# Optimization experiments

Measured on AMD Instinct MI355X. Metric: run time of the kernel, lower is better.

## Reference

```python
import jax, jax.numpy as jnp
import numpy as np

HEADS = 16
DIM_HEAD = 64
SCALE = DIM_HEAD ** -0.5


def setup_inputs() -> dict:
    key = jax.random.key(0)
    k1, k2, k3, k4 = jax.random.split(key, 4)
    b, n, dim = 2, 2048, 1024
    inner = HEADS * DIM_HEAD  # 1024
    x = jax.random.normal(k1, (b, n, dim), dtype=jnp.float32)
    # binary keep-mask (multiplicative, as in the original module)
    seq_mask = (jax.random.uniform(k2, (b, n)) < 0.9).astype(jnp.float32)
    # weights stored [in, out] (transpose of torch Linear layout)
    w_qkv = jax.random.normal(k3, (dim, inner * 3), dtype=jnp.float32) * (dim ** -0.5)
    w_out = jax.random.normal(k4, (inner, dim), dtype=jnp.float32) * (inner ** -0.5)
    return {"x": x, "seq_mask": seq_mask, "w_qkv": w_qkv, "w_out": w_out}


def reference(x, seq_mask, w_qkv, w_out):
    b, n, dim = x.shape
    qkv = x @ w_qkv                                   # [b, n, 3*inner]
    q, k, v = jnp.split(qkv, 3, axis=-1)
    split_heads = lambda t: t.reshape(b, n, HEADS, DIM_HEAD).transpose(0, 2, 1, 3)
    q, k, v = split_heads(q), split_heads(k), split_heads(v)  # [b, h, n, d]
    dots = jnp.einsum('bhid,bhjd->bhij', q, k) * SCALE        # [b, h, n, n]
    # multiplicative mask, broadcast over heads and query index i; mask depends on key index j
    dots = dots * seq_mask[:, None, None, :]
    attn = jax.nn.softmax(dots, axis=-1)
    out = jnp.einsum('bhij,bhjd->bhid', attn, v)              # [b, h, n, d]
    out = out.transpose(0, 2, 1, 3).reshape(b, n, HEADS * DIM_HEAD)
    return out @ w_out                                        # dropout p=0 -> identity
```

## Files before the change

### kernel.cpp

```cpp
#include <hip/hip_runtime.h>
#include <hip/hip_bf16.h>

using bf16 = __hip_bfloat16;
typedef __attribute__((ext_vector_type(8))) short short8;
typedef __attribute__((ext_vector_type(4))) float floatx4;
typedef __attribute__((ext_vector_type(16))) float floatx16;

#define MFMA_BF16(a, b, c) __builtin_amdgcn_mfma_f32_16x16x32_bf16((a), (b), (c), 0, 0, 0)
#define MFMA32(a, b, c) __builtin_amdgcn_mfma_f32_32x32x16_bf16((a), (b), (c), 0, 0, 0)

__device__ __forceinline__ void gload_lds16(const bf16* g, bf16* l) {
  __builtin_amdgcn_global_load_lds((__attribute__((address_space(1))) void*)g,
                                   (__attribute__((address_space(3))) void*)l,
                                   16, 0, 0);
}

__device__ __forceinline__ unsigned short bfbits(float f) {
  bf16 b = __float2bfloat16(f);
  return *reinterpret_cast<unsigned short*>(&b);
}

#define KSCALE 0.18033688011112042f

__global__ __launch_bounds__(256)
void probemask_k(const void* __restrict__ msrc, bf16* __restrict__ dst,
                 int* __restrict__ flag) {
  __shared__ int any;
  const int tid = threadIdx.x;
  if (tid == 0) any = 0;
  __syncthreads();
  const unsigned* mw = (const unsigned*)msrc;
  int bad = 0;
#pragma unroll
  for (int i = 0; i < 4; i++) {
    unsigned w = mw[tid * 4 + i];
    if (w != 0u && w != 0x3F800000u) bad = 1;
  }
  if (bad) atomicOr(&any, 1);
  __syncthreads();
  const int isbf = any;
  if (tid == 0) flag[0] = isbf;
  if (isbf) {
#pragma unroll
    for (int i = 0; i < 2; i++)
      ((int4*)dst)[tid * 2 + i] = ((const int4*)msrc)[tid * 2 + i];
  } else {
#pragma unroll
    for (int i = 0; i < 4; i++) {
      float4 v = ((const float4*)msrc)[tid * 4 + i];
      int o = tid * 16 + i * 4;
      dst[o + 0] = __float2bfloat16(v.x);
      dst[o + 1] = __float2bfloat16(v.y);
      dst[o + 2] = __float2bfloat16(v.z);
      dst[o + 3] = __float2bfloat16(v.w);
    }
  }
}

__global__ __launch_bounds__(256)
void cvt_k(const void* __restrict__ src, bf16* __restrict__ dst, int n,
           const int* __restrict__ flag) {
  if (*flag) return;
  int i = (blockIdx.x * 256 + threadIdx.x) * 4;
  if (i >= n) return;
  float4 v = ((const float4*)src)[i >> 2];
  dst[i + 0] = __float2bfloat16(v.x);
  dst[i + 1] = __float2bfloat16(v.y);
  dst[i + 2] = __float2bfloat16(v.z);
  dst[i + 3] = __float2bfloat16(v.w);
}

__global__ __launch_bounds__(256)
void transpose2_k(const void* __restrict__ in0, bf16* __restrict__ out0,
                  const void* __restrict__ in1, bf16* __restrict__ out1,
                  const int* __restrict__ flag) {
  __shared__ bf16 tile[32][33];
  const int isbf = *flag;
  constexpr int R = 1024;
  const void* in;
  bf16* out;
  int C, bx;
  if (blockIdx.x < 96) { in = in0; out = out0; C = 3072; bx = blockIdx.x * 32; }
  else                 { in = in1; out = out1; C = 1024; bx = (blockIdx.x - 96) * 32; }
  int by = blockIdx.y * 32;
  int tx = threadIdx.x & 31, ty = threadIdx.x >> 5;
#pragma unroll
  for (int i = 0; i < 4; i++) {
    size_t idx = (size_t)(by + ty + i * 8) * C + bx + tx;
    tile[ty + i * 8][tx] =
        isbf ? ((const bf16*)in)[idx] : __float2bfloat16(((const float*)in)[idx]);
  }
  __syncthreads();
#pragma unroll
  for (int i = 0; i < 4; i++)
    out[(size_t)(bx + ty + i * 8) * R + by + tx] = tile[tx][ty + i * 8];
}

template <int MODE>
__global__ __launch_bounds__(256, 2)
void gemm_k(const bf16* __restrict__ A, const bf16* __restrict__ Aalt,
            const bf16* __restrict__ Bt,
            bf16* __restrict__ Qo, bf16* __restrict__ Ko, bf16* __restrict__ Vo,
            void* __restrict__ Co, const bf16* __restrict__ Mk,
            const int* __restrict__ flag) {
  constexpr int K = 1024;
  __shared__ __align__(16) bf16 As[128 * 32];
  __shared__ __align__(16) bf16 Bs[128 * 32];

  const int tid = threadIdx.x;
  const int lane = tid & 63;
  const int wv = tid >> 6;
  const int wm = wv & 1, wn = wv >> 1;
  const int l15 = lane & 15, quad = lane >> 4;

  const int bm = blockIdx.y * 128;
  const int bn = blockIdx.x * 128;

  const int sml = tid >> 2;
  const int sg = (tid & 3) ^ ((sml >> 1) & 3);

  const int isbf = *flag;
  const bf16* Ab = (MODE == 0 && isbf) ? Aalt : A;

  floatx4 acc[4][4] = {};

  for (int k0 = 0; k0 < K; k0 += 32) {
    __syncthreads();
    const bf16* a0 = Ab + (size_t)(bm + sml) * K + k0 + sg * 8;
    gload_lds16(a0, &As[tid * 8]);
    gload_lds16(a0 + (size_t)64 * K, &As[2048 + tid * 8]);
    const bf16* b0 = Bt + (size_t)(bn + sml) * K + k0 + sg * 8;
    gload_lds16(b0, &Bs[tid * 8]);
    gload_lds16(b0 + (size_t)64 * K, &Bs[2048 + tid * 8]);
    __syncthreads();

    short8 af[4], bfr[4];
#pragma unroll
    for (int mi = 0; mi < 4; mi++) {
      int m = wm * 64 + mi * 16 + l15;
      af[mi] = *(const short8*)&As[m * 32 + ((quad ^ ((m >> 1) & 3)) * 8)];
    }
#pragma unroll
    for (int ni = 0; ni < 4; ni++) {
      int n = wn * 64 + ni * 16 + l15;
      bfr[ni] = *(const short8*)&Bs[n * 32 + ((quad ^ ((n >> 1) & 3)) * 8)];
    }
#pragma unroll
    for (int mi = 0; mi < 4; mi++)
#pragma unroll
      for (int ni = 0; ni < 4; ni++)
        acc[mi][ni] = MFMA_BF16(af[mi], bfr[ni], acc[mi][ni]);
  }

#pragma unroll
  for (int mi = 0; mi < 4; mi++) {
    const int row0 = bm + wm * 64 + mi * 16 + quad * 4;
#pragma unroll
    for (int ni = 0; ni < 4; ni++) {
      const int col = bn + wn * 64 + ni * 16 + l15;
      if (MODE == 0) {
        const int sec = col >> 10;
        const int cc = col & 1023;
        const int h = cc >> 6, d = cc & 63;
        const int b_idx = row0 >> 11;
        const int nn0 = row0 & 2047;
        if (sec == 0) {
          bf16* dst = Qo + (size_t)(b_idx * 16 + h) * 131072 + (size_t)nn0 * 64 + d;
#pragma unroll
          for (int r = 0; r < 4; r++) dst[r * 64] = __float2bfloat16(acc[mi][ni][r]);
        } else if (sec == 1) {
          const bf16* mrow = Mk + (size_t)b_idx * 2048 + nn0;
          const int t = nn0 >> 6, kt = (nn0 >> 5) & 1, l31r = nn0 & 31;
          const int g = d >> 3, j = d & 7;
          bf16* dst = Ko + (size_t)(b_idx * 16 + h) * 131072 + t * 4096 + kt * 2048 +
                      (g >> 1) * 512 + (g & 1) * 256 + l31r * 8 + j;
#pragma unroll
          for (int r = 0; r < 4; r++)
            dst[r * 8] = __float2bfloat16(acc[mi][ni][r] * KSCALE *
                                          __bfloat162float(mrow[r]));
        } else {
          const int t = nn0 >> 6;
          const int kl = nn0 & 63;
          const int g = kl >> 3, j0 = kl & 7;
          bf16* dst = Vo + (size_t)(b_idx * 16 + h) * 131072 + t * 4096 +
                      (d >> 5) * 2048 + (g >> 1) * 512 + (g & 1) * 256 + (d & 31) * 8 + j0;
          ushort4 u;
          u.x = bfbits(acc[mi][ni][0]);
          u.y = bfbits(acc[mi][ni][1]);
          u.z = bfbits(acc[mi][ni][2]);
          u.w = bfbits(acc[mi][ni][3]);
          *(ushort4*)dst = u;
        }
      } else {
        if (isbf) {
          bf16* C2 = (bf16*)Co;
#pragma unroll
          for (int r = 0; r < 4; r++)
            C2[(size_t)(row0 + r) * 1024 + col] = __float2bfloat16(acc[mi][ni][r]);
        } else {
          float* C2 = (float*)Co;
#pragma unroll
          for (int r = 0; r < 4; r++)
            C2[(size_t)(row0 + r) * 1024 + col] = acc[mi][ni][r];
        }
      }
    }
  }
}

__global__ __launch_bounds__(512, 4)
void flash_k(const bf16* __restrict__ Q, const bf16* __restrict__ Kp,
             const bf16* __restrict__ Vp, bf16* __restrict__ AO) {
  __shared__ __align__(16) float cb[4 * 64 * 32];
  __shared__ float rbuf[4 * 64];

  const int tid = threadIdx.x;
  const int lane = tid & 63;
  const int l31 = lane & 31;
  const int l5h = lane >> 5;
  const int w = tid >> 6;
  const int rg = w & 3;
  const int half = w >> 2;

  const int bid = blockIdx.x;
  const int wk = (bid & 7) * 64 + (bid >> 3);
  const int qt = wk & 15;
  const int hl = wk >> 4;
  const int b_idx = hl >> 4, h = hl & 15;

  const bf16* Qh = Q + (size_t)hl * 131072;
  const int lo = l5h * 256 + l31 * 8;
  const bf16* kptr = Kp + (size_t)hl * 131072 + (size_t)(half * 16) * 4096 + lo;
  const bf16* vptr = Vp + (size_t)hl * 131072 + (size_t)(half * 16) * 4096 + lo;

  const int qbase = qt * 128 + rg * 32;
  const int qrow = qbase + l31;

  short8 qf[4];
#pragma unroll
  for (int c = 0; c < 4; c++)
    qf[c] = *(const short8*)&Qh[(size_t)qrow * 64 + c * 16 + l5h * 8];

  floatx16 o_acc[2] = {};
  float rsum = 0.f;

  short8 kf[4];
#pragma unroll
  for (int c = 0; c < 4; c++) kf[c] = *(const short8*)(kptr + c * 512);

#pragma unroll 1
  for (int it = 0; it < 32; ++it) {
    const int kv = it & 1;

    floatx16 s = {};
    __builtin_amdgcn_s_setprio(1);
#pragma unroll
    for (int c = 0; c < 4; c++) s = MFMA32(kf[c], qf[c], s);
    __builtin_amdgcn_s_setprio(0);

    short8 vf[4];
#pragma unroll
    for (int dt = 0; dt < 2; dt++)
#pragma unroll
      for (int ch = 0; ch < 2; ch++)
        vf[dt * 2 + ch] = *(const short8*)(vptr + dt * 2048 + (kv * 2 + ch) * 512);

    kptr += (it < 31) ? 2048 : 0;
#pragma unroll
    for (int c = 0; c < 4; c++) kf[c] = *(const short8*)(kptr + c * 512);

    float rs0 = 0.f, rs1 = 0.f, rs2 = 0.f, rs3 = 0.f;
#pragma unroll
    for (int r = 0; r < 16; r += 4) {
      const float p0 = __builtin_amdgcn_exp2f(s[r + 0]);
      const float p1 = __builtin_amdgcn_exp2f(s[r + 1]);
      const float p2 = __builtin_amdgcn_exp2f(s[r + 2]);
      const float p3 = __builtin_amdgcn_exp2f(s[r + 3]);
      s[r + 0] = p0; rs0 += p0;
      s[r + 1] = p1; rs1 += p1;
      s[r + 2] = p2; rs2 += p2;
      s[r + 3] = p3; rs3 += p3;
    }
    float rs = (rs0 + rs1) + (rs2 + rs3);
    rs += __shfl_xor(rs, 32, 64);
    rsum += rs;

    short8 pf[2];
#pragma unroll
    for (int ch = 0; ch < 2; ch++) {
      const int rb = ch * 8;
      unsigned x0, x1, y0, y1;
      asm("v_cvt_pk_bf16_f32 %0, %1, %2" : "=v"(x0) : "v"(s[rb + 0]), "v"(s[rb + 1]));
      asm("v_cvt_pk_bf16_f32 %0, %1, %2" : "=v"(x1) : "v"(s[rb + 2]), "v"(s[rb + 3]));
      asm("v_cvt_pk_bf16_f32 %0, %1, %2" : "=v"(y0) : "v"(s[rb + 4]), "v"(s[rb + 5]));
      asm("v_cvt_pk_bf16_f32 %0, %1, %2" : "=v"(y1) : "v"(s[rb + 6]), "v"(s[rb + 7]));
      asm("v_permlane32_swap_b32 %0, %1" : "+v"(x0), "+v"(y0));
      asm("v_permlane32_swap_b32 %0, %1" : "+v"(x1), "+v"(y1));
      union { unsigned u[4]; short8 v; } cv;
      cv.u[0] = x0; cv.u[1] = x1; cv.u[2] = y0; cv.u[3] = y1;
      pf[ch] = cv.v;
    }

    __builtin_amdgcn_s_setprio(1);
#pragma unroll
    for (int dt = 0; dt < 2; dt++)
#pragma unroll
      for (int ch = 0; ch < 2; ch++)
        o_acc[dt] = MFMA32(vf[dt * 2 + ch], pf[ch], o_acc[dt]);
    __builtin_amdgcn_s_setprio(0);

    vptr += kv ? 4096 : 0;
  }

  if (w >= 4) {
    const int slot = (w - 4) * 64 + lane;
    float4* dst = (float4*)(cb + (size_t)slot * 32);
#pragma unroll
    for (int dt = 0; dt < 2; dt++)
#pragma unroll
      for (int q = 0; q < 4; q++) {
        float4 v = make_float4(o_acc[dt][q * 4 + 0], o_acc[dt][q * 4 + 1],
                               o_acc[dt][q * 4 + 2], o_acc[dt][q * 4 + 3]);
        dst[(dt * 4 + q) ^ (lane & 7)] = v;
      }
    rbuf[slot] = rsum;
  }
  __syncthreads();
  if (w < 4) {
    const int slot = w * 64 + lane;
    const float4* src = (const float4*)(cb + (size_t)slot * 32);
#pragma unroll
    for (int dt = 0; dt < 2; dt++)
#pragma unroll
      for (int q = 0; q < 4; q++) {
        float4 v = src[(dt * 4 + q) ^ (lane & 7)];
        o_acc[dt][q * 4 + 0] += v.x;
        o_acc[dt][q * 4 + 1] += v.y;
        o_acc[dt][q * 4 + 2] += v.z;
        o_acc[dt][q * 4 + 3] += v.w;
      }
    rsum += rbuf[slot];

    const float rinv = 1.f / rsum;
    bf16* orow = AO + (size_t)(b_idx * 2048 + qbase + l31) * 1024 + h * 64;
#pragma unroll
    for (int dt = 0; dt < 2; dt++)
#pragma unroll
      for (int rg2 = 0; rg2 < 4; rg2++) {
        ushort4 u;
        u.x = bfbits(o_acc[dt][rg2 * 4 + 0] * rinv);
        u.y = bfbits(o_acc[dt][rg2 * 4 + 1] * rinv);
        u.z = bfbits(o_acc[dt][rg2 * 4 + 2] * rinv);
        u.w = bfbits(o_acc[dt][rg2 * 4 + 3] * rinv);
        *(ushort4*)&orow[dt * 32 + rg2 * 8 + l5h * 4] = u;
      }
  }
}

extern "C" void kernel_launch(void* const* d_in, const int* in_sizes, int n_in,
                              void* d_out, int out_size, void* d_ws, size_t ws_size,
                              hipStream_t stream) {
  const void* x     = d_in[0];
  const void* mask  = d_in[1];
  const void* w_qkv = d_in[2];
  const void* w_out = d_in[3];

  bf16* ws    = (bf16*)d_ws;
  bf16* xb    = ws;
  bf16* AO    = ws;
  bf16* wqkvT = ws + 4194304;
  bf16* woutT = wqkvT + 3145728;
  bf16* Qb    = woutT + 1048576;
  bf16* Kp    = Qb + 4194304;
  bf16* maskb = Kp + 4194304;
  int*  flag  = (int*)(maskb + 4096);
  bf16* Vp    = (bf16*)d_out;

  probemask_k<<<1, 256, 0, stream>>>(mask, maskb, flag);
  cvt_k<<<4096, 256, 0, stream>>>(x, xb, 4194304, flag);
  transpose2_k<<<dim3(128, 32), 256, 0, stream>>>(w_qkv, wqkvT, w_out, woutT, flag);
  gemm_k<0><<<dim3(24, 32), 256, 0, stream>>>(xb, (const bf16*)x, wqkvT, Qb, Kp, Vp,
                                              nullptr, maskb, flag);
  flash_k<<<512, 512, 0, stream>>>(Qb, Kp, Vp, AO);
  gemm_k<1><<<dim3(8, 32), 256, 0, stream>>>(AO, nullptr, woutT, nullptr, nullptr,
                                             nullptr, d_out, nullptr, flag);
}
```

Baseline: 191.5 us.

## Merge prep kernels, swizzle GEMM block order, defer softmax row-sum reduction

Fuses the x-to-bf16 conversion and the weight transpose into one launch, removing a kernel launch and its serialization gap. Remaps GEMM workgroup IDs with an XCD-style interleave so neighbouring tiles share L2 on the same chiplet. In the flash kernel, the per-iteration row-sum reduction and cross-half shuffle move out of the loop into four running accumulators, reduced once at the end. This shortens the inner loop's dependency chain at the cost of a few extra registers and a separate exp buffer.

```diff
diff --git a/kernel.cpp b/kernel.cpp
--- a/kernel.cpp
+++ b/kernel.cpp
@@ -58,31 +58,31 @@
 }
 
 __global__ __launch_bounds__(256)
-void cvt_k(const void* __restrict__ src, bf16* __restrict__ dst, int n,
-           const int* __restrict__ flag) {
-  if (*flag) return;
-  int i = (blockIdx.x * 256 + threadIdx.x) * 4;
-  if (i >= n) return;
-  float4 v = ((const float4*)src)[i >> 2];
-  dst[i + 0] = __float2bfloat16(v.x);
-  dst[i + 1] = __float2bfloat16(v.y);
-  dst[i + 2] = __float2bfloat16(v.z);
-  dst[i + 3] = __float2bfloat16(v.w);
-}
-
-__global__ __launch_bounds__(256)
-void transpose2_k(const void* __restrict__ in0, bf16* __restrict__ out0,
-                  const void* __restrict__ in1, bf16* __restrict__ out1,
-                  const int* __restrict__ flag) {
+void prep_k(const void* __restrict__ xsrc, bf16* __restrict__ xb,
+            const void* __restrict__ in0, bf16* __restrict__ out0,
+            const void* __restrict__ in1, bf16* __restrict__ out1,
+            const int* __restrict__ flag) {
   __shared__ bf16 tile[32][33];
   const int isbf = *flag;
+  if (blockIdx.x < 4096) {
+    if (isbf) return;
+    int i = (blockIdx.x * 256 + threadIdx.x) * 4;
+    float4 v = ((const float4*)xsrc)[i >> 2];
+    xb[i + 0] = __float2bfloat16(v.x);
+    xb[i + 1] = __float2bfloat16(v.y);
+    xb[i + 2] = __float2bfloat16(v.z);
+    xb[i + 3] = __float2bfloat16(v.w);
+    return;
+  }
   constexpr int R = 1024;
+  const int t = blockIdx.x - 4096;
+  const int bxi = t & 127;
+  const int by = (t >> 7) * 32;
   const void* in;
   bf16* out;
   int C, bx;
-  if (blockIdx.x < 96) { in = in0; out = out0; C = 3072; bx = blockIdx.x * 32; }
-  else                 { in = in1; out = out1; C = 1024; bx = (blockIdx.x - 96) * 32; }
-  int by = blockIdx.y * 32;
+  if (bxi < 96) { in = in0; out = out0; C = 3072; bx = bxi * 32; }
+  else          { in = in1; out = out1; C = 1024; bx = (bxi - 96) * 32; }
   int tx = threadIdx.x & 31, ty = threadIdx.x >> 5;
 #pragma unroll
   for (int i = 0; i < 4; i++) {
@@ -113,8 +113,12 @@
   const int wm = wv & 1, wn = wv >> 1;
   const int l15 = lane & 15, quad = lane >> 4;
 
-  const int bm = blockIdx.y * 128;
-  const int bn = blockIdx.x * 128;
+  const int nbx = gridDim.x;
+  const int nwg = nbx * gridDim.y;
+  int wid = blockIdx.y * nbx + blockIdx.x;
+  wid = (wid & 7) * (nwg >> 3) + (wid >> 3);
+  const int bm = (wid / nbx) * 128;
+  const int bn = (wid % nbx) * 128;
 
   const int sml = tid >> 2;
   const int sg = (tid & 3) ^ ((sml >> 1) & 3);
@@ -242,7 +246,7 @@
     qf[c] = *(const short8*)&Qh[(size_t)qrow * 64 + c * 16 + l5h * 8];
 
   floatx16 o_acc[2] = {};
-  float rsum = 0.f;
+  float rsm0 = 0.f, rsm1 = 0.f, rsm2 = 0.f, rsm3 = 0.f;
 
   short8 kf[4];
 #pragma unroll
@@ -269,31 +273,28 @@
 #pragma unroll
     for (int c = 0; c < 4; c++) kf[c] = *(const short8*)(kptr + c * 512);
 
-    float rs0 = 0.f, rs1 = 0.f, rs2 = 0.f, rs3 = 0.f;
+    float e[16];
 #pragma unroll
     for (int r = 0; r < 16; r += 4) {
-      const float p0 = __builtin_amdgcn_exp2f(s[r + 0]);
-      const float p1 = __builtin_amdgcn_exp2f(s[r + 1]);
-      const float p2 = __builtin_amdgcn_exp2f(s[r + 2]);
-      const float p3 = __builtin_amdgcn_exp2f(s[r + 3]);
-      s[r + 0] = p0; rs0 += p0;
-      s[r + 1] = p1; rs1 += p1;
-      s[r + 2] = p2; rs2 += p2;
-      s[r + 3] = p3; rs3 += p3;
-    }
-    float rs = (rs0 + rs1) + (rs2 + rs3);
-    rs += __shfl_xor(rs, 32, 64);
-    rsum += rs;
+      e[r + 0] = __builtin_amdgcn_exp2f(s[r + 0]);
+      e[r + 1] = __builtin_amdgcn_exp2f(s[r + 1]);
+      e[r + 2] = __builtin_amdgcn_exp2f(s[r + 2]);
+      e[r + 3] = __builtin_amdgcn_exp2f(s[r + 3]);
+      rsm0 += e[r + 0];
+      rsm1 += e[r + 1];
+      rsm2 += e[r + 2];
+      rsm3 += e[r + 3];
+    }
 
     short8 pf[2];
 #pragma unroll
     for (int ch = 0; ch < 2; ch++) {
       const int rb = ch * 8;
       unsigned x0, x1, y0, y1;
-      asm("v_cvt_pk_bf16_f32 %0, %1, %2" : "=v"(x0) : "v"(s[rb + 0]), "v"(s[rb + 1]));
-      asm("v_cvt_pk_bf16_f32 %0, %1, %2" : "=v"(x1) : "v"(s[rb + 2]), "v"(s[rb + 3]));
-      asm("v_cvt_pk_bf16_f32 %0, %1, %2" : "=v"(y0) : "v"(s[rb + 4]), "v"(s[rb + 5]));
-      asm("v_cvt_pk_bf16_f32 %0, %1, %2" : "=v"(y1) : "v"(s[rb + 6]), "v"(s[rb + 7]));
+      asm("v_cvt_pk_bf16_f32 %0, %1, %2" : "=v"(x0) : "v"(e[rb + 0]), "v"(e[rb + 1]));
+      asm("v_cvt_pk_bf16_f32 %0, %1, %2" : "=v"(x1) : "v"(e[rb + 2]), "v"(e[rb + 3]));
+      asm("v_cvt_pk_bf16_f32 %0, %1, %2" : "=v"(y0) : "v"(e[rb + 4]), "v"(e[rb + 5]));
+      asm("v_cvt_pk_bf16_f32 %0, %1, %2" : "=v"(y1) : "v"(e[rb + 6]), "v"(e[rb + 7]));
       asm("v_permlane32_swap_b32 %0, %1" : "+v"(x0), "+v"(y0));
       asm("v_permlane32_swap_b32 %0, %1" : "+v"(x1), "+v"(y1));
       union { unsigned u[4]; short8 v; } cv;
@@ -311,6 +312,9 @@
 
     vptr += kv ? 4096 : 0;
   }
+
+  float rsum = (rsm0 + rsm1) + (rsm2 + rsm3);
+  rsum += __shfl_xor(rsum, 32, 64);
 
   if (w >= 4) {
     const int slot = (w - 4) * 64 + lane;
@@ -377,8 +381,7 @@
   bf16* Vp    = (bf16*)d_out;
 
   probemask_k<<<1, 256, 0, stream>>>(mask, maskb, flag);
-  cvt_k<<<4096, 256, 0, stream>>>(x, xb, 4194304, flag);
-  transpose2_k<<<dim3(128, 32), 256, 0, stream>>>(w_qkv, wqkvT, w_out, woutT, flag);
+  prep_k<<<8192, 256, 0, stream>>>(x, xb, w_qkv, wqkvT, w_out, woutT, flag);
   gemm_k<0><<<dim3(24, 32), 256, 0, stream>>>(xb, (const bf16*)x, wqkvT, Qb, Kp, Vp,
                                               nullptr, maskb, flag);
   flash_k<<<512, 512, 0, stream>>>(Qb, Kp, Vp, AO);
```

After: 188.6 us. Within noise of the previous version (-1.5%).
